# Optimization experiments

Measured on AMD Instinct MI355X. Metric: run time of the kernel, lower is better.

Reference implementation:

```python
import jax, jax.numpy as jnp
import numpy as np

B = 4194304  # batch
H = 32       # hidden width of TinyMLP


def _xavier(key, fan_in, fan_out, gain=0.5):
    lim = gain * np.sqrt(6.0 / (fan_in + fan_out))
    return jax.random.uniform(key, (fan_in, fan_out), jnp.float32, -lim, lim)


def setup_inputs() -> dict:
    key = jax.random.key(0)
    ks = jax.random.split(key, 7)
    return {
        "x1": jax.random.normal(ks[0], (B,), jnp.float32),
        "x2": jax.random.normal(ks[1], (B,), jnp.float32),
        "y1": jax.random.normal(ks[2], (B,), jnp.float32),
        "y2": jax.random.normal(ks[3], (B,), jnp.float32),
        "W1": _xavier(ks[4], 2, H),
        "b1": jnp.zeros((H,), jnp.float32),
        "W2": _xavier(ks[5], H, H),
        "b2": jnp.zeros((H,), jnp.float32),
        "W3": _xavier(ks[6], H, 1),
        "b3": jnp.zeros((1,), jnp.float32),
    }


def reference(x1, x2, y1, y2, W1, b1, W2, b2, W3, b3):
    # Y: [B, 2]
    Y = jnp.stack([y1, y2], axis=1)

    def F_sum(Yv):
        h1 = jax.nn.sigmoid(Yv @ W1 + b1)   # [B, H]
        h2 = jax.nn.sigmoid(h1 @ W2 + b2)   # [B, H]
        return jnp.sum(h2 @ W3 + b3)        # scalar sum of F values

    dF_dY = jax.grad(F_sum)(Y)              # [B, 2], analytic input-gradient

    x1_out = x1 + dF_dY[:, 0]
    x2_out = x2 + dF_dY[:, 1]
    # Stack the 4 output streams as columns: (x1', x2', y1, y2)
    return jnp.stack([x1_out, x2_out, y1, y2], axis=1)
```

## Files before the change

### kernel.cpp

```cpp
#include <hip/hip_runtime.h>


#define H 32
#define NLOG2E (-1.4426950408889634f)

typedef __attribute__((ext_vector_type(8))) short bf16x8;
typedef __attribute__((ext_vector_type(4))) float f32x4;
typedef __attribute__((ext_vector_type(2))) float f32x2;
typedef __attribute__((ext_vector_type(2))) __bf16 bfx2;

#define MFMA16 __builtin_amdgcn_mfma_f32_16x16x32_bf16

__device__ __forceinline__ int cvt_pk_bf16(float a, float b) {
    f32x2 f; f[0] = a; f[1] = b;
    bfx2 r = __builtin_convertvector(f, bfx2);
    return __builtin_bit_cast(int, r);
}
__device__ __forceinline__ unsigned f2bf(float f) {
    return (unsigned)cvt_pk_bf16(f, 0.f) & 0xFFFFu;
}
__device__ __forceinline__ float bf2f(unsigned s) {
    unsigned u = s << 16; return __builtin_bit_cast(float, u);
}
__device__ __forceinline__ float pklo(int p) {
    unsigned u = (unsigned)p << 16; return __builtin_bit_cast(float, u);
}
__device__ __forceinline__ float pkhi(int p) {
    unsigned u = (unsigned)p & 0xFFFF0000u; return __builtin_bit_cast(float, u);
}

__device__ __forceinline__ f32x4 rcp4(const f32x4 a) {
    float m01 = a[0] * a[1], m23 = a[2] * a[3];
    float r   = __builtin_amdgcn_rcpf(m01 * m23);
    float r01 = r * m23, r23 = r * m01;
    f32x4 s; s[0] = a[1] * r01; s[1] = a[0] * r01; s[2] = a[3] * r23; s[3] = a[2] * r23;
    return s;
}

__global__ __launch_bounds__(256, 8) void tinymlp_mfma_kernel(
    const float* __restrict__ x1, const float* __restrict__ x2,
    const float* __restrict__ y1, const float* __restrict__ y2,
    const float* __restrict__ W1, const float* __restrict__ b1,
    const float* __restrict__ W2, const float* __restrict__ b2,
    const float* __restrict__ W3,
    float4* __restrict__ out, int ntiles)
{
    __shared__ unsigned short lds0[4096];

    const int tid  = threadIdx.x;
    const int w    = tid >> 6;
    const int lane = tid & 63;
    const int m    = lane & 15;
    const int q    = lane >> 4;
    const int kb   = q * 8;

    bf16x8 bW2s_0, bW2s_1, bW2T3_0, bW2T3_1, bW1r;
    #pragma unroll
    for (int j = 0; j < 8; ++j) {
        bW2s_0[j] = (short)f2bf(NLOG2E * W2[(kb + j) * H + m]);
        bW2s_1[j] = (short)f2bf(NLOG2E * W2[(kb + j) * H + m + 16]);
        const float w3 = W3[kb + j];
        bW2T3_0[j] = (short)f2bf(W2[m * H + kb + j] * w3);
        bW2T3_1[j] = (short)f2bf(W2[(m + 16) * H + kb + j] * w3);
        bW1r[j] = (m < 2) ? (short)f2bf(W1[m * H + kb + j]) : (short)0;
    }

    union { int i[4]; bf16x8 v; } uW1lo, uW1hi;
    uW1lo.i[0] = uW1lo.i[1] = uW1lo.i[2] = uW1lo.i[3] = 0;
    uW1hi.i[0] = uW1hi.i[1] = uW1hi.i[2] = uW1hi.i[3] = 0;
    if (q == 0) {
        #pragma unroll
        for (int half = 0; half < 2; ++half) {
            const int h = m + 16 * half;
            const float wa = NLOG2E * W1[h];
            const float wb = NLOG2E * W1[H + h];
            const float bv = NLOG2E * b1[h];
            const unsigned ah = f2bf(wa), bh = f2bf(wb);
            const unsigned al = f2bf(wa - bf2f(ah)), bl = f2bf(wb - bf2f(bh));
            const unsigned ch = f2bf(bv);
            const unsigned cl = f2bf(bv - bf2f(ch));
            int i0 = (int)(ah | (bh << 16));
            int i1 = (int)(al | (bl << 16));
            int i3 = (int)(ch | (cl << 16));
            if (half == 0) { uW1lo.i[0] = i0; uW1lo.i[1] = i1; uW1lo.i[2] = i0; uW1lo.i[3] = i3; }
            else           { uW1hi.i[0] = i0; uW1hi.i[1] = i1; uW1hi.i[2] = i0; uW1hi.i[3] = i3; }
        }
    }

    f32x4 b2C0, b2C1;
    {
        const float4 t0 = ((const float4*)b2)[q];
        const float4 t1 = ((const float4*)b2)[q + 4];
        b2C0[0] = NLOG2E * t0.x; b2C0[1] = NLOG2E * t0.y; b2C0[2] = NLOG2E * t0.z; b2C0[3] = NLOG2E * t0.w;
        b2C1[0] = NLOG2E * t1.x; b2C1[1] = NLOG2E * t1.y; b2C1[2] = NLOG2E * t1.z; b2C1[3] = NLOG2E * t1.w;
    }

    unsigned short*       wp = &lds0[w * 1024 + (q >> 1) * 128 + m * 8 + (q & 1) * 4];
    const unsigned short* rp = &lds0[w * 1024 + lane * 8];

    const int gwave  = (blockIdx.x * blockDim.x + tid) >> 6;
    const int nwaves = (gridDim.x * blockDim.x) >> 6;
    unsigned idx = (unsigned)gwave * 16 + (unsigned)m;
    const unsigned step = (unsigned)nwaves * 16;

    for (int tile = gwave; tile < ntiles; tile += nwaves) {
        const float y1v = y1[idx];
        const float y2v = y2[idx];
        float xv1 = 0.f, xv2 = 0.f;
        if (lane < 16) { xv1 = x1[idx]; xv2 = x2[idx]; }

        const int pkHI = cvt_pk_bf16(y1v, y2v);
        const float l1 = y1v - pklo(pkHI);
        const float l2 = y2v - pkhi(pkHI);
        const int pkLO = cvt_pk_bf16(l1, l2);
        union { int i[4]; bf16x8 v; } uY;
        uY.i[0] = pkHI; uY.i[1] = pkHI; uY.i[2] = pkLO; uY.i[3] = 0x3F803F80;

        const f32x4 zf = {0.f, 0.f, 0.f, 0.f};

        f32x4 zL = MFMA16(uW1lo.v, uY.v, zf, 0, 0, 0);
        f32x4 zH = MFMA16(uW1hi.v, uY.v, zf, 0, 0, 0);

        f32x4 aL, aH;
        #pragma unroll
        for (int r = 0; r < 4; ++r) {
            aL[r] = __builtin_amdgcn_exp2f(zL[r]);
            aH[r] = __builtin_amdgcn_exp2f(zH[r]);
        }
        aL += 1.0f; aH += 1.0f;
        const f32x4 sL = rcp4(aL);
        const f32x4 sH = rcp4(aH);
        const int P0 = cvt_pk_bf16(sL[0], sL[1]);
        const int P1 = cvt_pk_bf16(sL[2], sL[3]);
        const int P2 = cvt_pk_bf16(sH[0], sH[1]);
        const int P3 = cvt_pk_bf16(sH[2], sH[3]);

        int2 wv0; wv0.x = P0; wv0.y = P1;
        int2 wv1; wv1.x = P2; wv1.y = P3;
        *(int2*)wp         = wv0;
        *(int2*)(wp + 256) = wv1;
        __builtin_amdgcn_wave_barrier();
        const bf16x8 uaH = *(const bf16x8*)rp;

        f32x4 zzL = MFMA16(bW2s_0, uaH, b2C0, 0, 0, 0);
        f32x4 zzH = MFMA16(bW2s_1, uaH, b2C1, 0, 0, 0);

        f32x4 cL, cH;
        #pragma unroll
        for (int r = 0; r < 4; ++r) {
            cL[r] = __builtin_amdgcn_exp2f(zzL[r]);
            cH[r] = __builtin_amdgcn_exp2f(zzH[r]);
        }
        cL += 1.0f; cH += 1.0f;
        const f32x4 s2L = rcp4(cL);
        const f32x4 s2H = rcp4(cH);
        f32x2 d0; d0[0] = s2L[0]; d0[1] = s2L[1]; d0 = __builtin_elementwise_fma(-d0, d0, d0);
        f32x2 d1; d1[0] = s2L[2]; d1[1] = s2L[3]; d1 = __builtin_elementwise_fma(-d1, d1, d1);
        f32x2 d2; d2[0] = s2H[0]; d2[1] = s2H[1]; d2 = __builtin_elementwise_fma(-d2, d2, d2);
        f32x2 d3; d3[0] = s2H[2]; d3[1] = s2H[3]; d3 = __builtin_elementwise_fma(-d3, d3, d3);

        int2 qv0; qv0.x = cvt_pk_bf16(d0[0], d0[1]); qv0.y = cvt_pk_bf16(d1[0], d1[1]);
        int2 qv1; qv1.x = cvt_pk_bf16(d2[0], d2[1]); qv1.y = cvt_pk_bf16(d3[0], d3[1]);
        *(int2*)(wp + 512) = qv0;
        *(int2*)(wp + 768) = qv1;
        __builtin_amdgcn_wave_barrier();
        const bf16x8 aD = *(const bf16x8*)(rp + 512);

        f32x4 dLo = MFMA16(bW2T3_0, aD, zf, 0, 0, 0);
        f32x4 dHi = MFMA16(bW2T3_1, aD, zf, 0, 0, 0);

        f32x2 sv, gg;
        sv[0] = pklo(P0); sv[1] = pkhi(P0);
        f32x2 h0 = __builtin_elementwise_fma(-sv, sv, sv);
        gg[0] = dLo[0]; gg[1] = dLo[1]; gg *= h0;
        const int G0 = cvt_pk_bf16(gg[0], gg[1]);
        sv[0] = pklo(P1); sv[1] = pkhi(P1);
        h0 = __builtin_elementwise_fma(-sv, sv, sv);
        gg[0] = dLo[2]; gg[1] = dLo[3]; gg *= h0;
        const int G1 = cvt_pk_bf16(gg[0], gg[1]);
        sv[0] = pklo(P2); sv[1] = pkhi(P2);
        h0 = __builtin_elementwise_fma(-sv, sv, sv);
        gg[0] = dHi[0]; gg[1] = dHi[1]; gg *= h0;
        const int G2 = cvt_pk_bf16(gg[0], gg[1]);
        sv[0] = pklo(P3); sv[1] = pkhi(P3);
        h0 = __builtin_elementwise_fma(-sv, sv, sv);
        gg[0] = dHi[2]; gg[1] = dHi[3]; gg *= h0;
        const int G3 = cvt_pk_bf16(gg[0], gg[1]);

        int2 gv0; gv0.x = G0; gv0.y = G1;
        int2 gv1; gv1.x = G2; gv1.y = G3;
        *(int2*)wp         = gv0;
        *(int2*)(wp + 256) = gv1;
        __builtin_amdgcn_wave_barrier();
        const bf16x8 uaG = *(const bf16x8*)rp;

        f32x4 accY = MFMA16(bW1r, uaG, zf, 0, 0, 0);

        if (lane < 16) {
            float4 o;
            o.x = xv1 + accY[0];
            o.y = xv2 + accY[1];
            o.z = y1v;
            o.w = y2v;
            out[idx] = o;
        }
        __builtin_amdgcn_wave_barrier();
        idx += step;
    }
}

extern "C" void kernel_launch(void* const* d_in, const int* in_sizes, int n_in,
                              void* d_out, int out_size, void* d_ws, size_t ws_size,
                              hipStream_t stream) {
    const float* x1 = (const float*)d_in[0];
    const float* x2 = (const float*)d_in[1];
    const float* y1 = (const float*)d_in[2];
    const float* y2 = (const float*)d_in[3];
    const float* W1 = (const float*)d_in[4];
    const float* b1 = (const float*)d_in[5];
    const float* W2 = (const float*)d_in[6];
    const float* b2 = (const float*)d_in[7];
    const float* W3 = (const float*)d_in[8];

    const int n = in_sizes[0];
    const int ntiles = n / 16;
    const int block = 256;
    const int grid = 2048;
    tinymlp_mfma_kernel<<<grid, block, 0, stream>>>(
        x1, x2, y1, y2, W1, b1, W2, b2, W3, (float4*)d_out, ntiles);
}
```

Measured before the change: 212.5 us.

## Process two tiles per wave iteration to interleave independent MFMA chains

Each wave now handles a pair of 16-row tiles per loop iteration, with separate LDS buffers, so each stage runs for both tiles back to back and the independent MFMA, exp and rcp chains can overlap latency. The x loads are deferred until after stage 2 to shorten live ranges. To fit the extra registers and LDS, launch bounds drop from 8 to 6 waves-per-EU occupancy and the grid shrinks from 2048 to 1536 blocks. This trades occupancy for instruction-level parallelism, and it assumes ntiles is even, since an odd final tile would be skipped.

```diff
diff --git a/kernel.cpp b/kernel.cpp
--- a/kernel.cpp
+++ b/kernel.cpp
@@ -37,7 +37,7 @@
     return s;
 }
 
-__global__ __launch_bounds__(256, 8) void tinymlp_mfma_kernel(
+__global__ __launch_bounds__(256, 6) void tinymlp_mfma_kernel(
     const float* __restrict__ x1, const float* __restrict__ x2,
     const float* __restrict__ y1, const float* __restrict__ y2,
     const float* __restrict__ W1, const float* __restrict__ b1,
@@ -45,7 +45,7 @@
     const float* __restrict__ W3,
     float4* __restrict__ out, int ntiles)
 {
-    __shared__ unsigned short lds0[4096];
+    __shared__ unsigned short lds0[8192];
 
     const int tid  = threadIdx.x;
     const int w    = tid >> 6;
@@ -95,32 +95,23 @@
         b2C1[0] = NLOG2E * t1.x; b2C1[1] = NLOG2E * t1.y; b2C1[2] = NLOG2E * t1.z; b2C1[3] = NLOG2E * t1.w;
     }
 
-    unsigned short*       wp = &lds0[w * 1024 + (q >> 1) * 128 + m * 8 + (q & 1) * 4];
-    const unsigned short* rp = &lds0[w * 1024 + lane * 8];
-
-    const int gwave  = (blockIdx.x * blockDim.x + tid) >> 6;
-    const int nwaves = (gridDim.x * blockDim.x) >> 6;
-    unsigned idx = (unsigned)gwave * 16 + (unsigned)m;
-    const unsigned step = (unsigned)nwaves * 16;
-
-    for (int tile = gwave; tile < ntiles; tile += nwaves) {
-        const float y1v = y1[idx];
-        const float y2v = y2[idx];
-        float xv1 = 0.f, xv2 = 0.f;
-        if (lane < 16) { xv1 = x1[idx]; xv2 = x2[idx]; }
-
+    const int woff = (q >> 1) * 128 + m * 8 + (q & 1) * 4;
+    unsigned short*       wpA = &lds0[w * 2048 + woff];
+    unsigned short*       wpB = &lds0[w * 2048 + 1024 + woff];
+    const unsigned short* rpA = &lds0[w * 2048 + lane * 8];
+    const unsigned short* rpB = &lds0[w * 2048 + 1024 + lane * 8];
+
+    const f32x4 zf = {0.f, 0.f, 0.f, 0.f};
+
+    auto stage1 = [&](float y1v, float y2v, unsigned short* wp, int* P) {
         const int pkHI = cvt_pk_bf16(y1v, y2v);
         const float l1 = y1v - pklo(pkHI);
         const float l2 = y2v - pkhi(pkHI);
         const int pkLO = cvt_pk_bf16(l1, l2);
         union { int i[4]; bf16x8 v; } uY;
         uY.i[0] = pkHI; uY.i[1] = pkHI; uY.i[2] = pkLO; uY.i[3] = 0x3F803F80;
-
-        const f32x4 zf = {0.f, 0.f, 0.f, 0.f};
-
         f32x4 zL = MFMA16(uW1lo.v, uY.v, zf, 0, 0, 0);
         f32x4 zH = MFMA16(uW1hi.v, uY.v, zf, 0, 0, 0);
-
         f32x4 aL, aH;
         #pragma unroll
         for (int r = 0; r < 4; ++r) {
@@ -130,21 +121,20 @@
         aL += 1.0f; aH += 1.0f;
         const f32x4 sL = rcp4(aL);
         const f32x4 sH = rcp4(aH);
-        const int P0 = cvt_pk_bf16(sL[0], sL[1]);
-        const int P1 = cvt_pk_bf16(sL[2], sL[3]);
-        const int P2 = cvt_pk_bf16(sH[0], sH[1]);
-        const int P3 = cvt_pk_bf16(sH[2], sH[3]);
-
-        int2 wv0; wv0.x = P0; wv0.y = P1;
-        int2 wv1; wv1.x = P2; wv1.y = P3;
+        P[0] = cvt_pk_bf16(sL[0], sL[1]);
+        P[1] = cvt_pk_bf16(sL[2], sL[3]);
+        P[2] = cvt_pk_bf16(sH[0], sH[1]);
+        P[3] = cvt_pk_bf16(sH[2], sH[3]);
+        int2 wv0; wv0.x = P[0]; wv0.y = P[1];
+        int2 wv1; wv1.x = P[2]; wv1.y = P[3];
         *(int2*)wp         = wv0;
         *(int2*)(wp + 256) = wv1;
-        __builtin_amdgcn_wave_barrier();
+    };
+
+    auto stage2 = [&](const unsigned short* rp, unsigned short* wp) {
         const bf16x8 uaH = *(const bf16x8*)rp;
-
         f32x4 zzL = MFMA16(bW2s_0, uaH, b2C0, 0, 0, 0);
         f32x4 zzH = MFMA16(bW2s_1, uaH, b2C1, 0, 0, 0);
-
         f32x4 cL, cH;
         #pragma unroll
         for (int r = 0; r < 4; ++r) {
@@ -158,53 +148,88 @@
         f32x2 d1; d1[0] = s2L[2]; d1[1] = s2L[3]; d1 = __builtin_elementwise_fma(-d1, d1, d1);
         f32x2 d2; d2[0] = s2H[0]; d2[1] = s2H[1]; d2 = __builtin_elementwise_fma(-d2, d2, d2);
         f32x2 d3; d3[0] = s2H[2]; d3[1] = s2H[3]; d3 = __builtin_elementwise_fma(-d3, d3, d3);
-
         int2 qv0; qv0.x = cvt_pk_bf16(d0[0], d0[1]); qv0.y = cvt_pk_bf16(d1[0], d1[1]);
         int2 qv1; qv1.x = cvt_pk_bf16(d2[0], d2[1]); qv1.y = cvt_pk_bf16(d3[0], d3[1]);
         *(int2*)(wp + 512) = qv0;
         *(int2*)(wp + 768) = qv1;
-        __builtin_amdgcn_wave_barrier();
+    };
+
+    auto stage3 = [&](const unsigned short* rp, unsigned short* wp, const int* P) {
         const bf16x8 aD = *(const bf16x8*)(rp + 512);
-
         f32x4 dLo = MFMA16(bW2T3_0, aD, zf, 0, 0, 0);
         f32x4 dHi = MFMA16(bW2T3_1, aD, zf, 0, 0, 0);
-
-        f32x2 sv, gg;
-        sv[0] = pklo(P0); sv[1] = pkhi(P0);
-        f32x2 h0 = __builtin_elementwise_fma(-sv, sv, sv);
+        f32x2 sv, gg, h0;
+        sv[0] = pklo(P[0]); sv[1] = pkhi(P[0]);
+        h0 = __builtin_elementwise_fma(-sv, sv, sv);
         gg[0] = dLo[0]; gg[1] = dLo[1]; gg *= h0;
         const int G0 = cvt_pk_bf16(gg[0], gg[1]);
-        sv[0] = pklo(P1); sv[1] = pkhi(P1);
+        sv[0] = pklo(P[1]); sv[1] = pkhi(P[1]);
         h0 = __builtin_elementwise_fma(-sv, sv, sv);
         gg[0] = dLo[2]; gg[1] = dLo[3]; gg *= h0;
         const int G1 = cvt_pk_bf16(gg[0], gg[1]);
-        sv[0] = pklo(P2); sv[1] = pkhi(P2);
+        sv[0] = pklo(P[2]); sv[1] = pkhi(P[2]);
         h0 = __builtin_elementwise_fma(-sv, sv, sv);
         gg[0] = dHi[0]; gg[1] = dHi[1]; gg *= h0;
         const int G2 = cvt_pk_bf16(gg[0], gg[1]);
-        sv[0] = pklo(P3); sv[1] = pkhi(P3);
+        sv[0] = pklo(P[3]); sv[1] = pkhi(P[3]);
         h0 = __builtin_elementwise_fma(-sv, sv, sv);
         gg[0] = dHi[2]; gg[1] = dHi[3]; gg *= h0;
         const int G3 = cvt_pk_bf16(gg[0], gg[1]);
-
         int2 gv0; gv0.x = G0; gv0.y = G1;
         int2 gv1; gv1.x = G2; gv1.y = G3;
         *(int2*)wp         = gv0;
         *(int2*)(wp + 256) = gv1;
-        __builtin_amdgcn_wave_barrier();
+    };
+
+    auto stage4 = [&](const unsigned short* rp, float xv1, float xv2,
+                      float yv1, float yv2, unsigned oidx) {
         const bf16x8 uaG = *(const bf16x8*)rp;
-
         f32x4 accY = MFMA16(bW1r, uaG, zf, 0, 0, 0);
-
         if (lane < 16) {
             float4 o;
             o.x = xv1 + accY[0];
             o.y = xv2 + accY[1];
-            o.z = y1v;
-            o.w = y2v;
-            out[idx] = o;
-        }
-        __builtin_amdgcn_wave_barrier();
+            o.z = yv1;
+            o.w = yv2;
+            out[oidx] = o;
+        }
+    };
+
+    const int gpair  = (blockIdx.x * blockDim.x + tid) >> 6;
+    const int nwaves = (gridDim.x * blockDim.x) >> 6;
+    const int npairs = ntiles >> 1;
+    unsigned idx = (unsigned)gpair * 32 + (unsigned)m;
+    const unsigned step = (unsigned)nwaves * 32;
+
+    for (int p = gpair; p < npairs; p += nwaves) {
+        const float yA1 = y1[idx];
+        const float yA2 = y2[idx];
+        const float yB1 = y1[idx + 16];
+        const float yB2 = y2[idx + 16];
+
+        int PA[4], PB[4];
+        stage1(yA1, yA2, wpA, PA);
+        stage1(yB1, yB2, wpB, PB);
+        __builtin_amdgcn_wave_barrier();
+
+        stage2(rpA, wpA);
+        stage2(rpB, wpB);
+        __builtin_amdgcn_wave_barrier();
+
+        float xA1 = 0.f, xA2 = 0.f, xB1 = 0.f, xB2 = 0.f;
+        if (lane < 16) {
+            xA1 = x1[idx];      xA2 = x2[idx];
+            xB1 = x1[idx + 16]; xB2 = x2[idx + 16];
+        }
+
+        stage3(rpA, wpA, PA);
+        stage3(rpB, wpB, PB);
+        __builtin_amdgcn_wave_barrier();
+
+        stage4(rpA, xA1, xA2, yA1, yA2, idx);
+        stage4(rpB, xB1, xB2, yB1, yB2, idx + 16);
+        __builtin_amdgcn_wave_barrier();
+
         idx += step;
     }
 }
@@ -225,7 +250,7 @@
     const int n = in_sizes[0];
     const int ntiles = n / 16;
     const int block = 256;
-    const int grid = 2048;
+    const int grid = 1536;
     tinymlp_mfma_kernel<<<grid, block, 0, stream>>>(
         x1, x2, y1, y2, W1, b1, W2, b2, W3, (float4*)d_out, ntiles);
 }
```

Result: no change. 214.6 us (+1.0%).

## Switch TinyMLP tiles from 16x16x32 to 32x32x16 MFMA with 32-sample tiles

Applied to the files above, without the earlier changes.

Restructures the per-wave tile from 16 samples to 32 samples and replaces the 16x16x32 bf16 MFMAs with 32x32x16 bf16 MFMAs. This lowers MFMA issue count per sample, since the first layer needs one MFMA instead of two. The LDS staging layout is reorganized and doubled to match the 32x32 output layout, and the grid and launch-bounds occupancy are lowered. In exchange, only half the lanes load and store the sample data, each lane uses more registers, and fewer waves are resident to hide memory latency.

```diff
diff --git a/kernel.cpp b/kernel.cpp
--- a/kernel.cpp
+++ b/kernel.cpp
@@ -5,22 +5,17 @@
 #define NLOG2E (-1.4426950408889634f)
 
 typedef __attribute__((ext_vector_type(8))) short bf16x8;
+typedef __attribute__((ext_vector_type(16))) float f32x16;
 typedef __attribute__((ext_vector_type(4))) float f32x4;
 typedef __attribute__((ext_vector_type(2))) float f32x2;
 typedef __attribute__((ext_vector_type(2))) __bf16 bfx2;
 
-#define MFMA16 __builtin_amdgcn_mfma_f32_16x16x32_bf16
+#define MFMA32 __builtin_amdgcn_mfma_f32_32x32x16_bf16
 
 __device__ __forceinline__ int cvt_pk_bf16(float a, float b) {
     f32x2 f; f[0] = a; f[1] = b;
     bfx2 r = __builtin_convertvector(f, bfx2);
     return __builtin_bit_cast(int, r);
-}
-__device__ __forceinline__ unsigned f2bf(float f) {
-    return (unsigned)cvt_pk_bf16(f, 0.f) & 0xFFFFu;
-}
-__device__ __forceinline__ float bf2f(unsigned s) {
-    unsigned u = s << 16; return __builtin_bit_cast(float, u);
 }
 __device__ __forceinline__ float pklo(int p) {
     unsigned u = (unsigned)p << 16; return __builtin_bit_cast(float, u);
@@ -37,7 +32,7 @@
     return s;
 }
 
-__global__ __launch_bounds__(256, 8) void tinymlp_mfma_kernel(
+__global__ __launch_bounds__(256, 6) void tinymlp_mfma_kernel(
     const float* __restrict__ x1, const float* __restrict__ x2,
     const float* __restrict__ y1, const float* __restrict__ y2,
     const float* __restrict__ W1, const float* __restrict__ b1,
@@ -45,166 +40,151 @@
     const float* __restrict__ W3,
     float4* __restrict__ out, int ntiles)
 {
-    __shared__ unsigned short lds0[4096];
+    __shared__ unsigned short lds0[8192];
 
     const int tid  = threadIdx.x;
     const int w    = tid >> 6;
     const int lane = tid & 63;
-    const int m    = lane & 15;
-    const int q    = lane >> 4;
-    const int kb   = q * 8;
-
-    bf16x8 bW2s_0, bW2s_1, bW2T3_0, bW2T3_1, bW1r;
+    const int n    = lane & 31;
+    const int q5   = lane >> 5;
+
+    union U4 { int i[4]; bf16x8 v; };
+    U4 A_z1, A_z2a, A_z2b, A_dh1a, A_dh1b, A_dya, A_dyb;
+
     #pragma unroll
-    for (int j = 0; j < 8; ++j) {
-        bW2s_0[j] = (short)f2bf(NLOG2E * W2[(kb + j) * H + m]);
-        bW2s_1[j] = (short)f2bf(NLOG2E * W2[(kb + j) * H + m + 16]);
-        const float w3 = W3[kb + j];
-        bW2T3_0[j] = (short)f2bf(W2[m * H + kb + j] * w3);
-        bW2T3_1[j] = (short)f2bf(W2[(m + 16) * H + kb + j] * w3);
-        bW1r[j] = (m < 2) ? (short)f2bf(W1[m * H + kb + j]) : (short)0;
-    }
-
-    union { int i[4]; bf16x8 v; } uW1lo, uW1hi;
-    uW1lo.i[0] = uW1lo.i[1] = uW1lo.i[2] = uW1lo.i[3] = 0;
-    uW1hi.i[0] = uW1hi.i[1] = uW1hi.i[2] = uW1hi.i[3] = 0;
-    if (q == 0) {
-        #pragma unroll
-        for (int half = 0; half < 2; ++half) {
-            const int h = m + 16 * half;
-            const float wa = NLOG2E * W1[h];
-            const float wb = NLOG2E * W1[H + h];
-            const float bv = NLOG2E * b1[h];
-            const unsigned ah = f2bf(wa), bh = f2bf(wb);
-            const unsigned al = f2bf(wa - bf2f(ah)), bl = f2bf(wb - bf2f(bh));
-            const unsigned ch = f2bf(bv);
-            const unsigned cl = f2bf(bv - bf2f(ch));
-            int i0 = (int)(ah | (bh << 16));
-            int i1 = (int)(al | (bl << 16));
-            int i3 = (int)(ch | (cl << 16));
-            if (half == 0) { uW1lo.i[0] = i0; uW1lo.i[1] = i1; uW1lo.i[2] = i0; uW1lo.i[3] = i3; }
-            else           { uW1hi.i[0] = i0; uW1hi.i[1] = i1; uW1hi.i[2] = i0; uW1hi.i[3] = i3; }
-        }
-    }
-
-    f32x4 b2C0, b2C1;
-    {
-        const float4 t0 = ((const float4*)b2)[q];
-        const float4 t1 = ((const float4*)b2)[q + 4];
-        b2C0[0] = NLOG2E * t0.x; b2C0[1] = NLOG2E * t0.y; b2C0[2] = NLOG2E * t0.z; b2C0[3] = NLOG2E * t0.w;
-        b2C1[0] = NLOG2E * t1.x; b2C1[1] = NLOG2E * t1.y; b2C1[2] = NLOG2E * t1.z; b2C1[3] = NLOG2E * t1.w;
-    }
-
-    unsigned short*       wp = &lds0[w * 1024 + (q >> 1) * 128 + m * 8 + (q & 1) * 4];
-    const unsigned short* rp = &lds0[w * 1024 + lane * 8];
+    for (int t = 0; t < 4; ++t) {
+        const int j0 = 8 * q5 + 2 * t;
+        const int j1 = j0 + 1;
+        A_z2a.i[t] = cvt_pk_bf16(NLOG2E * W2[j0 * H + n],        NLOG2E * W2[j1 * H + n]);
+        A_z2b.i[t] = cvt_pk_bf16(NLOG2E * W2[(16 + j0) * H + n], NLOG2E * W2[(16 + j1) * H + n]);
+        A_dh1a.i[t] = cvt_pk_bf16(W2[n * H + j0] * W3[j0],           W2[n * H + j1] * W3[j1]);
+        A_dh1b.i[t] = cvt_pk_bf16(W2[n * H + 16 + j0] * W3[16 + j0], W2[n * H + 16 + j1] * W3[16 + j1]);
+        A_dya.i[t] = (n < 2) ? cvt_pk_bf16(W1[n * H + j0],      W1[n * H + j1])      : 0;
+        A_dyb.i[t] = (n < 2) ? cvt_pk_bf16(W1[n * H + 16 + j0], W1[n * H + 16 + j1]) : 0;
+    }
+
+    A_z1.i[0] = A_z1.i[1] = A_z1.i[2] = A_z1.i[3] = 0;
+    if (q5 == 0) {
+        const float wa = NLOG2E * W1[n];
+        const float wb = NLOG2E * W1[H + n];
+        const float bv = NLOG2E * b1[n];
+        const int hi  = cvt_pk_bf16(wa, wb);
+        const int lo  = cvt_pk_bf16(wa - pklo(hi), wb - pkhi(hi));
+        const int bh  = cvt_pk_bf16(bv, 0.f);
+        const int bhl = cvt_pk_bf16(bv, bv - pklo(bh));
+        A_z1.i[0] = hi; A_z1.i[1] = lo; A_z1.i[2] = hi; A_z1.i[3] = bhl;
+    }
+
+    f32x16 b2C;
+    #pragma unroll
+    for (int t = 0; t < 4; ++t) {
+        const float4 bt = *(const float4*)&b2[8 * t + 4 * q5];
+        b2C[4 * t + 0] = NLOG2E * bt.x; b2C[4 * t + 1] = NLOG2E * bt.y;
+        b2C[4 * t + 2] = NLOG2E * bt.z; b2C[4 * t + 3] = NLOG2E * bt.w;
+    }
+
+    f32x16 zf16;
+    #pragma unroll
+    for (int r = 0; r < 16; ++r) zf16[r] = 0.f;
+
+    unsigned short*       wb = &lds0[w * 2048 + n * 8 + q5 * 4];
+    const unsigned short* rb = &lds0[w * 2048 + q5 * 256 + n * 8];
 
     const int gwave  = (blockIdx.x * blockDim.x + tid) >> 6;
     const int nwaves = (gridDim.x * blockDim.x) >> 6;
-    unsigned idx = (unsigned)gwave * 16 + (unsigned)m;
-    const unsigned step = (unsigned)nwaves * 16;
-
-    for (int tile = gwave; tile < ntiles; tile += nwaves) {
-        const float y1v = y1[idx];
-        const float y2v = y2[idx];
+    unsigned idx = (unsigned)gwave * 32 + (unsigned)n;
+    const unsigned step = (unsigned)nwaves * 32;
+
+    for (int tt = gwave; tt < ntiles; tt += nwaves) {
+        float y1v = 0.f, y2v = 0.f;
+        if (lane < 32) { y1v = y1[idx]; y2v = y2[idx]; }
+
+        U4 uY;
+        const int pkHI = cvt_pk_bf16(y1v, y2v);
+        const int pkLO = cvt_pk_bf16(y1v - pklo(pkHI), y2v - pkhi(pkHI));
+        uY.i[0] = pkHI; uY.i[1] = pkHI; uY.i[2] = pkLO;
+        uY.i[3] = (lane < 32) ? 0x3F803F80 : 0;
+
+        const f32x16 acc = MFMA32(A_z1.v, uY.v, zf16, 0, 0, 0);
+
+        int P[8];
+        #pragma unroll
+        for (int t = 0; t < 4; ++t) {
+            f32x4 e;
+            #pragma unroll
+            for (int r = 0; r < 4; ++r) e[r] = __builtin_amdgcn_exp2f(acc[4 * t + r]);
+            e += 1.0f;
+            const f32x4 s = rcp4(e);
+            P[2 * t]     = cvt_pk_bf16(s[0], s[1]);
+            P[2 * t + 1] = cvt_pk_bf16(s[2], s[3]);
+            int2 v; v.x = P[2 * t]; v.y = P[2 * t + 1];
+            *(int2*)(wb + t * 256) = v;
+        }
+        __builtin_amdgcn_wave_barrier();
+
+        const bf16x8 B1 = *(const bf16x8*)rb;
+        const bf16x8 B2 = *(const bf16x8*)(rb + 512);
+        f32x16 zz = MFMA32(A_z2a.v, B1, b2C, 0, 0, 0);
+        zz = MFMA32(A_z2b.v, B2, zz, 0, 0, 0);
+
+        #pragma unroll
+        for (int t = 0; t < 4; ++t) {
+            f32x4 e;
+            #pragma unroll
+            for (int r = 0; r < 4; ++r) e[r] = __builtin_amdgcn_exp2f(zz[4 * t + r]);
+            e += 1.0f;
+            const f32x4 s = rcp4(e);
+            f32x2 sv;
+            sv[0] = s[0]; sv[1] = s[1];
+            sv = __builtin_elementwise_fma(-sv, sv, sv);
+            const int q0 = cvt_pk_bf16(sv[0], sv[1]);
+            sv[0] = s[2]; sv[1] = s[3];
+            sv = __builtin_elementwise_fma(-sv, sv, sv);
+            const int q1 = cvt_pk_bf16(sv[0], sv[1]);
+            int2 v; v.x = q0; v.y = q1;
+            *(int2*)(wb + 1024 + t * 256) = v;
+        }
+        __builtin_amdgcn_wave_barrier();
+
         float xv1 = 0.f, xv2 = 0.f;
-        if (lane < 16) { xv1 = x1[idx]; xv2 = x2[idx]; }
-
-        const int pkHI = cvt_pk_bf16(y1v, y2v);
-        const float l1 = y1v - pklo(pkHI);
-        const float l2 = y2v - pkhi(pkHI);
-        const int pkLO = cvt_pk_bf16(l1, l2);
-        union { int i[4]; bf16x8 v; } uY;
-        uY.i[0] = pkHI; uY.i[1] = pkHI; uY.i[2] = pkLO; uY.i[3] = 0x3F803F80;
-
-        const f32x4 zf = {0.f, 0.f, 0.f, 0.f};
-
-        f32x4 zL = MFMA16(uW1lo.v, uY.v, zf, 0, 0, 0);
-        f32x4 zH = MFMA16(uW1hi.v, uY.v, zf, 0, 0, 0);
-
-        f32x4 aL, aH;
+        if (lane < 32) { xv1 = x1[idx]; xv2 = x2[idx]; }
+
+        const bf16x8 D1 = *(const bf16x8*)(rb + 1024);
+        const bf16x8 D2 = *(const bf16x8*)(rb + 1536);
+        f32x16 dh = MFMA32(A_dh1a.v, D1, zf16, 0, 0, 0);
+        dh = MFMA32(A_dh1b.v, D2, dh, 0, 0, 0);
+
         #pragma unroll
-        for (int r = 0; r < 4; ++r) {
-            aL[r] = __builtin_amdgcn_exp2f(zL[r]);
-            aH[r] = __builtin_amdgcn_exp2f(zH[r]);
-        }
-        aL += 1.0f; aH += 1.0f;
-        const f32x4 sL = rcp4(aL);
-        const f32x4 sH = rcp4(aH);
-        const int P0 = cvt_pk_bf16(sL[0], sL[1]);
-        const int P1 = cvt_pk_bf16(sL[2], sL[3]);
-        const int P2 = cvt_pk_bf16(sH[0], sH[1]);
-        const int P3 = cvt_pk_bf16(sH[2], sH[3]);
-
-        int2 wv0; wv0.x = P0; wv0.y = P1;
-        int2 wv1; wv1.x = P2; wv1.y = P3;
-        *(int2*)wp         = wv0;
-        *(int2*)(wp + 256) = wv1;
-        __builtin_amdgcn_wave_barrier();
-        const bf16x8 uaH = *(const bf16x8*)rp;
-
-        f32x4 zzL = MFMA16(bW2s_0, uaH, b2C0, 0, 0, 0);
-        f32x4 zzH = MFMA16(bW2s_1, uaH, b2C1, 0, 0, 0);
-
-        f32x4 cL, cH;
-        #pragma unroll
-        for (int r = 0; r < 4; ++r) {
-            cL[r] = __builtin_amdgcn_exp2f(zzL[r]);
-            cH[r] = __builtin_amdgcn_exp2f(zzH[r]);
-        }
-        cL += 1.0f; cH += 1.0f;
-        const f32x4 s2L = rcp4(cL);
-        const f32x4 s2H = rcp4(cH);
-        f32x2 d0; d0[0] = s2L[0]; d0[1] = s2L[1]; d0 = __builtin_elementwise_fma(-d0, d0, d0);
-        f32x2 d1; d1[0] = s2L[2]; d1[1] = s2L[3]; d1 = __builtin_elementwise_fma(-d1, d1, d1);
-        f32x2 d2; d2[0] = s2H[0]; d2[1] = s2H[1]; d2 = __builtin_elementwise_fma(-d2, d2, d2);
-        f32x2 d3; d3[0] = s2H[2]; d3[1] = s2H[3]; d3 = __builtin_elementwise_fma(-d3, d3, d3);
-
-        int2 qv0; qv0.x = cvt_pk_bf16(d0[0], d0[1]); qv0.y = cvt_pk_bf16(d1[0], d1[1]);
-        int2 qv1; qv1.x = cvt_pk_bf16(d2[0], d2[1]); qv1.y = cvt_pk_bf16(d3[0], d3[1]);
-        *(int2*)(wp + 512) = qv0;
-        *(int2*)(wp + 768) = qv1;
-        __builtin_amdgcn_wave_barrier();
-        const bf16x8 aD = *(const bf16x8*)(rp + 512);
-
-        f32x4 dLo = MFMA16(bW2T3_0, aD, zf, 0, 0, 0);
-        f32x4 dHi = MFMA16(bW2T3_1, aD, zf, 0, 0, 0);
-
-        f32x2 sv, gg;
-        sv[0] = pklo(P0); sv[1] = pkhi(P0);
-        f32x2 h0 = __builtin_elementwise_fma(-sv, sv, sv);
-        gg[0] = dLo[0]; gg[1] = dLo[1]; gg *= h0;
-        const int G0 = cvt_pk_bf16(gg[0], gg[1]);
-        sv[0] = pklo(P1); sv[1] = pkhi(P1);
-        h0 = __builtin_elementwise_fma(-sv, sv, sv);
-        gg[0] = dLo[2]; gg[1] = dLo[3]; gg *= h0;
-        const int G1 = cvt_pk_bf16(gg[0], gg[1]);
-        sv[0] = pklo(P2); sv[1] = pkhi(P2);
-        h0 = __builtin_elementwise_fma(-sv, sv, sv);
-        gg[0] = dHi[0]; gg[1] = dHi[1]; gg *= h0;
-        const int G2 = cvt_pk_bf16(gg[0], gg[1]);
-        sv[0] = pklo(P3); sv[1] = pkhi(P3);
-        h0 = __builtin_elementwise_fma(-sv, sv, sv);
-        gg[0] = dHi[2]; gg[1] = dHi[3]; gg *= h0;
-        const int G3 = cvt_pk_bf16(gg[0], gg[1]);
-
-        int2 gv0; gv0.x = G0; gv0.y = G1;
-        int2 gv1; gv1.x = G2; gv1.y = G3;
-        *(int2*)wp         = gv0;
-        *(int2*)(wp + 256) = gv1;
-        __builtin_amdgcn_wave_barrier();
-        const bf16x8 uaG = *(const bf16x8*)rp;
-
-        f32x4 accY = MFMA16(bW1r, uaG, zf, 0, 0, 0);
-
-        if (lane < 16) {
+        for (int t = 0; t < 4; ++t) {
+            f32x2 sv, gg;
+            sv[0] = pklo(P[2 * t]); sv[1] = pkhi(P[2 * t]);
+            sv = __builtin_elementwise_fma(-sv, sv, sv);
+            gg[0] = dh[4 * t]; gg[1] = dh[4 * t + 1]; gg *= sv;
+            const int g0 = cvt_pk_bf16(gg[0], gg[1]);
+            sv[0] = pklo(P[2 * t + 1]); sv[1] = pkhi(P[2 * t + 1]);
+            sv = __builtin_elementwise_fma(-sv, sv, sv);
+            gg[0] = dh[4 * t + 2]; gg[1] = dh[4 * t + 3]; gg *= sv;
+            const int g1 = cvt_pk_bf16(gg[0], gg[1]);
+            int2 v; v.x = g0; v.y = g1;
+            *(int2*)(wb + t * 256) = v;
+        }
+        __builtin_amdgcn_wave_barrier();
+
+        const bf16x8 E1 = *(const bf16x8*)rb;
+        const bf16x8 E2 = *(const bf16x8*)(rb + 512);
+        f32x16 ay = MFMA32(A_dya.v, E1, zf16, 0, 0, 0);
+        ay = MFMA32(A_dyb.v, E2, ay, 0, 0, 0);
+
+        if (lane < 32) {
             float4 o;
-            o.x = xv1 + accY[0];
-            o.y = xv2 + accY[1];
+            o.x = xv1 + ay[0];
+            o.y = xv2 + ay[1];
             o.z = y1v;
             o.w = y2v;
             out[idx] = o;
         }
         __builtin_amdgcn_wave_barrier();
+
         idx += step;
     }
 }
@@ -223,9 +203,9 @@
     const float* W3 = (const float*)d_in[8];
 
     const int n = in_sizes[0];
-    const int ntiles = n / 16;
+    const int ntiles = n / 32;
     const int block = 256;
-    const int grid = 2048;
+    const int grid = 1536;
     tinymlp_mfma_kernel<<<grid, block, 0, stream>>>(
         x1, x2, y1, y2, W1, b1, W2, b2, W3, (float4*)d_out, ntiles);
 }
```

Measured after the change: 203.9 us. -4.0%, faster.
